# Optimization experiments

Measured on AMD Instinct MI355X. Metric: run time of the kernel, lower is better.

## Reference

```python
import jax, jax.numpy as jnp
import numpy as np

B, H, W, C = 8, 64, 64, 512
CK, CV = C // 8, C // 2  # 64, 256


def maxpool2x2(x):
    # x: [B, H, W, C] -> [B, H//2, W//2, C], 2x2 max pool, stride 2 (keras MaxPooling2D default)
    b, h, w, c = x.shape
    return x.reshape(b, h // 2, 2, w // 2, 2, c).max(axis=(2, 4))


def setup_inputs() -> dict:
    key = jax.random.key(0)
    ks = jax.random.split(key, 6)
    wscale = 0.02
    return {
        "x": jax.random.normal(ks[0], (B, H, W, C), dtype=jnp.float32),
        "w_theta": jax.random.normal(ks[1], (C, CK), dtype=jnp.float32) * wscale,
        "w_phi": jax.random.normal(ks[2], (C, CK), dtype=jnp.float32) * wscale,
        "w_g": jax.random.normal(ks[3], (C, CV), dtype=jnp.float32) * wscale,
        "w_o": jax.random.normal(ks[4], (CV, C), dtype=jnp.float32) * wscale,
        "gamma": jax.random.normal(ks[5], (1,), dtype=jnp.float32),
    }


def reference(x, w_theta, w_phi, w_g, w_o, gamma):
    b, h, w, c = x.shape
    hw = h * w
    # theta: 1x1 conv -> [B, HW, C//8]
    theta = jnp.einsum('bhwc,ck->bhwk', x, w_theta).reshape(b, hw, -1)
    # phi: 1x1 conv + 2x2 maxpool -> [B, HW//4, C//8]
    phi = maxpool2x2(jnp.einsum('bhwc,ck->bhwk', x, w_phi)).reshape(b, hw // 4, -1)
    # attention: [B, HW, HW//4], softmax over last axis
    attn = jax.nn.softmax(jnp.einsum('bqk,bpk->bqp', theta, phi), axis=-1)
    # g: 1x1 conv + 2x2 maxpool -> [B, HW//4, C//2]
    g = maxpool2x2(jnp.einsum('bhwc,cv->bhwv', x, w_g)).reshape(b, hw // 4, -1)
    # attn_g: [B, HW, C//2] -> [B, H, W, C//2] -> 1x1 conv -> [B, H, W, C]
    attn_g = jnp.einsum('bqp,bpv->bqv', attn, g).reshape(b, h, w, -1)
    attn_g = jnp.einsum('bhwv,vc->bhwc', attn_g, w_o)
    return x + gamma * attn_g
```

## Files before the change

### kernel.cpp

```cpp
#include <hip/hip_runtime.h>
#include <hip/hip_bf16.h>
#include <cstddef>
#include <cstdint>


typedef __attribute__((ext_vector_type(8))) short short8;
typedef __attribute__((ext_vector_type(4))) float float4v;

namespace {
constexpr int kB = 8, kC = 512, kCK = 64, kCV = 256, kHW = 4096, kP = 1024;
constexpr int kNP = 384;
}

__device__ __forceinline__ void gll16(const void* g, void* l) {
  __builtin_amdgcn_global_load_lds((uint32_t __attribute__((address_space(1)))*)g,
                                   (uint32_t __attribute__((address_space(3)))*)l,
                                   16, 0, 0);
}
__device__ __forceinline__ float4v mfma16(short8 a, short8 b, float4v c) {
  return __builtin_amdgcn_mfma_f32_16x16x32_bf16(a, b, c, 0, 0, 0);
}
__device__ __forceinline__ const short8* fragp(const char* tile, int row, int oct) {
  return (const short8*)(tile + row * 128 + ((oct ^ (row & 7)) * 16));
}
__device__ __forceinline__ const short8* fragp16(const char* tile, int row, int oct) {
  return (const short8*)(tile + row * 256 + ((oct ^ (row & 15)) * 16));
}

__global__ __launch_bounds__(256) void k_pack_w(
    const float* __restrict__ wt, const float* __restrict__ wphi,
    const float* __restrict__ wg, const float* __restrict__ wo,
    __hip_bfloat16* __restrict__ wAll, __hip_bfloat16* __restrict__ woT) {
  int idx = blockIdx.x * 256 + threadIdx.x;
  if (idx < 196608) {
    int n = idx >> 9, k = idx & 511;
    float v = (n < 64) ? wt[k * 64 + n]
            : (n < 128) ? wphi[k * 64 + (n - 64)]
                        : wg[k * 256 + (n - 128)];
    wAll[idx] = __float2bfloat16(v);
  } else {
    int t = idx - 196608;
    int n = t >> 8, k = t & 255;
    woT[t] = __float2bfloat16(wo[k * 512 + n]);
  }
}

__global__ __launch_bounds__(256) void k_proj(const float* __restrict__ x,
                                              const __hip_bfloat16* __restrict__ wAll,
                                              __hip_bfloat16* __restrict__ pgf) {
  __shared__ __align__(16) char smem[16384 + 49152];
  char* As = smem;
  char* Bs = smem + 16384;
  const int tid = threadIdx.x, wid = tid >> 6, lane = tid & 63;
  const int m = lane & 15, quad = lane >> 4;
  const int row0 = blockIdx.x * 64;
  const int wm = (wid >> 1) * 32, wn = (wid & 1) * 192;
  float4v acc[2][12] = {};
  for (int kc = 0; kc < 512; kc += 64) {
#pragma unroll
    for (int u = 0; u < 4; ++u) {
      const int r0 = (wid * 4 + u) * 4;
      const int row = r0 + (lane >> 4);
      const int sqg = (lane & 15) ^ (row & 15);
      gll16(x + (size_t)(row0 + row) * 512 + kc + sqg * 4, As + r0 * 256);
    }
#pragma unroll
    for (int u = 0; u < 12; ++u) {
      const int r0 = (wid * 12 + u) * 8;
      const int row = r0 + (lane >> 3);
      const int og = (lane & 7) ^ (row & 7);
      gll16(wAll + (size_t)row * 512 + kc + og * 8, Bs + r0 * 128);
    }
    __syncthreads();
#pragma unroll
    for (int kk = 0; kk < 64; kk += 32) {
      short8 af[2];
#pragma unroll
      for (int i = 0; i < 2; ++i) {
        const int row = wm + i * 16 + m;
        const int sq0 = (kk >> 2) + quad * 2;
        float4v lo = *(const float4v*)(As + row * 256 + ((sq0 ^ m) * 16));
        float4v hi = *(const float4v*)(As + row * 256 + (((sq0 + 1) ^ m) * 16));
        short8 a;
        a[0] = __builtin_bit_cast(short, __float2bfloat16(lo[0]));
        a[1] = __builtin_bit_cast(short, __float2bfloat16(lo[1]));
        a[2] = __builtin_bit_cast(short, __float2bfloat16(lo[2]));
        a[3] = __builtin_bit_cast(short, __float2bfloat16(lo[3]));
        a[4] = __builtin_bit_cast(short, __float2bfloat16(hi[0]));
        a[5] = __builtin_bit_cast(short, __float2bfloat16(hi[1]));
        a[6] = __builtin_bit_cast(short, __float2bfloat16(hi[2]));
        a[7] = __builtin_bit_cast(short, __float2bfloat16(hi[3]));
        af[i] = a;
      }
      const int oct = (kk >> 3) + quad;
#pragma unroll
      for (int j = 0; j < 12; ++j) {
        short8 bf = *fragp(Bs, wn + j * 16 + m, oct);
#pragma unroll
        for (int i = 0; i < 2; ++i) acc[i][j] = mfma16(af[i], bf, acc[i][j]);
      }
    }
    __syncthreads();
  }
#pragma unroll
  for (int i = 0; i < 2; ++i)
#pragma unroll
    for (int j = 0; j < 12; ++j)
#pragma unroll
      for (int r = 0; r < 4; ++r)
        pgf[(size_t)(row0 + wm + i * 16 + quad * 4 + r) * 384 + wn + j * 16 + m] =
            __float2bfloat16(acc[i][j][r]);
}

__global__ __launch_bounds__(256) void k_pool_phi(const __hip_bfloat16* __restrict__ pg,
                                                  __hip_bfloat16* __restrict__ phi_p) {
  int idx = blockIdx.x * 256 + threadIdx.x;
  int c = idx & 63;
  int p = (idx >> 6) & 1023;
  int b = idx >> 16;
  int ph = p >> 5, pw = p & 31;
  size_t base = ((size_t)b * 4096 + ph * 128 + pw * 2) * kNP + 64 + c;
  float v0 = __bfloat162float(pg[base]);
  float v1 = __bfloat162float(pg[base + kNP]);
  float v2 = __bfloat162float(pg[base + kNP * 64]);
  float v3 = __bfloat162float(pg[base + kNP * 64 + kNP]);
  phi_p[idx] = __float2bfloat16(fmaxf(fmaxf(v0, v1), fmaxf(v2, v3)));
}

__global__ __launch_bounds__(256) void k_pool_gT(const __hip_bfloat16* __restrict__ pg,
                                                 __hip_bfloat16* __restrict__ gT) {
  __shared__ __hip_bfloat16 t[64][65];
  const int p0 = blockIdx.x * 64, v0 = blockIdx.y * 64, b = blockIdx.z;
#pragma unroll
  for (int it = 0; it < 16; ++it) {
    int li = it * 256 + threadIdx.x;
    int pp = li >> 6, v = li & 63;
    int p = p0 + pp;
    int ph = p >> 5, pw = p & 31;
    size_t base = ((size_t)b * 4096 + ph * 128 + pw * 2) * kNP + 128 + v0 + v;
    float mv = fmaxf(
        fmaxf(__bfloat162float(pg[base]), __bfloat162float(pg[base + kNP])),
        fmaxf(__bfloat162float(pg[base + kNP * 64]), __bfloat162float(pg[base + kNP * 64 + kNP])));
    t[pp][v] = __float2bfloat16(mv);
  }
  __syncthreads();
#pragma unroll
  for (int it = 0; it < 16; ++it) {
    int li = it * 256 + threadIdx.x;
    int v = li >> 6, p = li & 63;
    gT[((size_t)b * 256 + v0 + v) * 1024 + p0 + p] = t[p][v];
  }
}

__global__ __launch_bounds__(512) void k_fattn(
    const __hip_bfloat16* __restrict__ pgf,
    const __hip_bfloat16* __restrict__ phip,
    const __hip_bfloat16* __restrict__ gT,
    __hip_bfloat16* __restrict__ O) {
  __shared__ __align__(16) char smem[65536 + 8192 + 1024 + 128];
  char* KG = smem;
  char* PQ = smem + 65536;
  float* pred = (float*)(smem + 65536 + 8192);
  float* rowstat = (float*)(smem + 65536 + 8192 + 1024);

  const int tid = threadIdx.x, wid = tid >> 6, lane = tid & 63;
  const int m = lane & 15, quad = lane >> 4;
  const int b = blockIdx.y, q0 = blockIdx.x * 32;

  if (wid < 4) {
    const int row = wid * 8 + (lane >> 3);
    const int og = (lane & 7) ^ (row & 7);
    gll16(pgf + (size_t)(b * kHW + q0 + row) * kNP + og * 8, PQ + wid * 8 * 128);
  }
  const __hip_bfloat16* phb = phip + (size_t)b * kP * 64;
  auto stageK = [&](int c, int buf) {
#pragma unroll
    for (int u = 0; u < 4; ++u) {
      const int r0 = wid * 32 + u * 8;
      const int row = r0 + (lane >> 3);
      const int og = (lane & 7) ^ (row & 7);
      gll16(phb + (size_t)(c * 256 + row) * 64 + og * 8, KG + buf * 32768 + r0 * 128);
    }
  };
  stageK(0, 0);
  __syncthreads();

  float4v sc[2][8] = {};
#pragma unroll
  for (int c = 0; c < 4; ++c) {
    if (c < 3) stageK(c + 1, (c + 1) & 1);
    const char* Kb = KG + (c & 1) * 32768;
    __builtin_amdgcn_s_setprio(1);
#pragma unroll
    for (int kk = 0; kk < 64; kk += 32) {
      const int oct = (kk >> 3) + quad;
      short8 a[2], bb[2];
#pragma unroll
      for (int i = 0; i < 2; ++i) a[i] = *fragp(PQ, i * 16 + m, oct);
#pragma unroll
      for (int j = 0; j < 2; ++j) bb[j] = *fragp(Kb, wid * 32 + j * 16 + m, oct);
#pragma unroll
      for (int i = 0; i < 2; ++i)
#pragma unroll
        for (int j = 0; j < 2; ++j) sc[i][c * 2 + j] = mfma16(a[i], bb[j], sc[i][c * 2 + j]);
    }
    __builtin_amdgcn_s_setprio(0);
    __syncthreads();
  }

  float mx[2][4];
#pragma unroll
  for (int i = 0; i < 2; ++i)
#pragma unroll
    for (int r = 0; r < 4; ++r) {
      float v = sc[i][0][r];
#pragma unroll
      for (int s = 1; s < 8; ++s) v = fmaxf(v, sc[i][s][r]);
#pragma unroll
      for (int d = 1; d < 16; d <<= 1) v = fmaxf(v, __shfl_xor(v, d));
      mx[i][r] = v;
    }
  if (m == 0) {
#pragma unroll
    for (int i = 0; i < 2; ++i)
#pragma unroll
      for (int r = 0; r < 4; ++r) pred[(i * 16 + quad * 4 + r) * 8 + wid] = mx[i][r];
  }
  __syncthreads();
  if (tid < 32) {
    float v = pred[tid * 8];
#pragma unroll
    for (int w = 1; w < 8; ++w) v = fmaxf(v, pred[tid * 8 + w]);
    rowstat[tid] = v;
  }
  __syncthreads();
  float sm[2][4];
#pragma unroll
  for (int i = 0; i < 2; ++i)
#pragma unroll
    for (int r = 0; r < 4; ++r) {
      const float rm = rowstat[i * 16 + quad * 4 + r];
      float s = 0.f;
#pragma unroll
      for (int ss = 0; ss < 8; ++ss) {
        float e = __expf(sc[i][ss][r] - rm);
        sc[i][ss][r] = e;
        s += e;
      }
#pragma unroll
      for (int d = 1; d < 16; d <<= 1) s += __shfl_xor(s, d);
      sm[i][r] = s;
    }
  __syncthreads();
  if (m == 0) {
#pragma unroll
    for (int i = 0; i < 2; ++i)
#pragma unroll
      for (int r = 0; r < 4; ++r) pred[(i * 16 + quad * 4 + r) * 8 + wid] = sm[i][r];
  }
  __syncthreads();
  if (tid < 32) {
    float s = 0.f;
#pragma unroll
    for (int w = 0; w < 8; ++w) s += pred[tid * 8 + w];
    rowstat[tid] = 1.f / s;
  }

  const __hip_bfloat16* gb = gT + (size_t)b * kCV * kP;
  auto stageG = [&](int cp, int buf) {
#pragma unroll
    for (int u = 0; u < 4; ++u) {
      const int r0 = wid * 32 + u * 8;
      const int row = r0 + (lane >> 3);
      const int og = (lane & 7) ^ (row & 7);
      gll16(gb + (size_t)row * kP + cp * 64 + og * 8, KG + buf * 32768 + r0 * 128);
    }
  };
  auto writePs = [&](int cp, int buf) {
    if ((wid >> 1) != (cp & 3)) return;
    const int c = cp >> 2;
    char* Pb = PQ + buf * 4096;
#pragma unroll
    for (int i = 0; i < 2; ++i)
#pragma unroll
      for (int jl = 0; jl < 2; ++jl) {
        const int pl = (wid & 1) * 32 + jl * 16 + m;
#pragma unroll
        for (int r = 0; r < 4; ++r) {
          const int row = i * 16 + quad * 4 + r;
          *(__hip_bfloat16*)(Pb + row * 128 + (((pl >> 3) ^ (row & 7)) * 16) +
                             (pl & 7) * 2) = __float2bfloat16(sc[i][c * 2 + jl][r]);
        }
      }
  };

  float4v oc[2][2] = {};
  stageG(0, 0);
  writePs(0, 0);
  __syncthreads();
  for (int cp = 0; cp < 16; ++cp) {
    const int cur = cp & 1;
    if (cp < 15) {
      stageG(cp + 1, cur ^ 1);
      writePs(cp + 1, cur ^ 1);
    }
    const char* Gb = KG + cur * 32768;
    const char* Pb = PQ + cur * 4096;
    __builtin_amdgcn_s_setprio(1);
#pragma unroll
    for (int kk = 0; kk < 64; kk += 32) {
      const int oct = (kk >> 3) + quad;
      short8 a[2], bb[2];
#pragma unroll
      for (int i = 0; i < 2; ++i) a[i] = *fragp(Pb, i * 16 + m, oct);
#pragma unroll
      for (int j = 0; j < 2; ++j) bb[j] = *fragp(Gb, wid * 32 + j * 16 + m, oct);
#pragma unroll
      for (int i = 0; i < 2; ++i)
#pragma unroll
        for (int j = 0; j < 2; ++j) oc[i][j] = mfma16(a[i], bb[j], oc[i][j]);
    }
    __builtin_amdgcn_s_setprio(0);
    __syncthreads();
  }
#pragma unroll
  for (int i = 0; i < 2; ++i)
#pragma unroll
    for (int j = 0; j < 2; ++j)
#pragma unroll
      for (int r = 0; r < 4; ++r) {
        const int row = i * 16 + quad * 4 + r;
        O[((size_t)b * kHW + q0 + row) * kCV + wid * 32 + j * 16 + m] =
            __float2bfloat16(oc[i][j][r] * rowstat[row]);
      }
}

__global__ __launch_bounds__(256) void k_out(const __hip_bfloat16* __restrict__ A,
                                             const __hip_bfloat16* __restrict__ Bw,
                                             const float* __restrict__ x,
                                             const float* __restrict__ gamma,
                                             float* __restrict__ out) {
  __shared__ __align__(16) char smem[4 * 16384];
  const int tid = threadIdx.x, wid = tid >> 6, lane = tid & 63;
  const int m = lane & 15, quad = lane >> 4;
  const int row0 = blockIdx.x * 128, col0 = blockIdx.y * 128;
  const int wm = (wid >> 1) * 64, wn = (wid & 1) * 64;
  float4v acc[4][4] = {};
  auto stage = [&](int t, int buf) {
    const int kc = t * 64;
#pragma unroll
    for (int u = 0; u < 4; ++u) {
      const int r0 = (wid * 4 + u) * 8;
      const int row = r0 + (lane >> 3);
      const int og = (lane & 7) ^ (row & 7);
      gll16(A + (size_t)(row0 + row) * 256 + kc + og * 8, smem + buf * 16384 + r0 * 128);
      gll16(Bw + (size_t)(col0 + row) * 256 + kc + og * 8,
            smem + 32768 + buf * 16384 + r0 * 128);
    }
  };
  stage(0, 0);
  __syncthreads();
#pragma unroll
  for (int t = 0; t < 4; ++t) {
    if (t < 3) stage(t + 1, (t + 1) & 1);
    const char* Ab = smem + (t & 1) * 16384;
    const char* Bb = smem + 32768 + (t & 1) * 16384;
    __builtin_amdgcn_s_setprio(1);
#pragma unroll
    for (int kk = 0; kk < 64; kk += 32) {
      const int oct = (kk >> 3) + quad;
      short8 af[4], bf[4];
#pragma unroll
      for (int i = 0; i < 4; ++i) af[i] = *fragp(Ab, wm + i * 16 + m, oct);
#pragma unroll
      for (int j = 0; j < 4; ++j) bf[j] = *fragp(Bb, wn + j * 16 + m, oct);
#pragma unroll
      for (int i = 0; i < 4; ++i)
#pragma unroll
        for (int j = 0; j < 4; ++j) acc[i][j] = mfma16(af[i], bf[j], acc[i][j]);
    }
    __builtin_amdgcn_s_setprio(0);
    __syncthreads();
  }
  const float g = gamma[0];
#pragma unroll
  for (int i = 0; i < 4; ++i)
#pragma unroll
    for (int j = 0; j < 4; ++j) {
      const int cc = col0 + wn + j * 16 + m;
      const int rb = row0 + wm + i * 16 + quad * 4;
#pragma unroll
      for (int r = 0; r < 4; ++r) {
        const size_t idx = (size_t)(rb + r) * 512 + cc;
        out[idx] = x[idx] + g * acc[i][j][r];
      }
    }
}

extern "C" void kernel_launch(void* const* d_in, const int* in_sizes, int n_in,
                              void* d_out, int out_size, void* d_ws, size_t ws_size,
                              hipStream_t stream) {
  (void)in_sizes; (void)n_in; (void)out_size; (void)ws_size;
  const float* x     = (const float*)d_in[0];
  const float* wt    = (const float*)d_in[1];
  const float* wphi  = (const float*)d_in[2];
  const float* wg    = (const float*)d_in[3];
  const float* wo    = (const float*)d_in[4];
  const float* gamma = (const float*)d_in[5];
  float* out = (float*)d_out;

  char* ws = (char*)d_ws;
  __hip_bfloat16* wAll = (__hip_bfloat16*)(ws);
  __hip_bfloat16* woT  = (__hip_bfloat16*)(ws + 393216);
  __hip_bfloat16* pgf  = (__hip_bfloat16*)(ws + 655360);
  __hip_bfloat16* phip = (__hip_bfloat16*)(ws + 25821184);
  __hip_bfloat16* gT   = (__hip_bfloat16*)(ws + 26869760);
  __hip_bfloat16* O    = (__hip_bfloat16*)(ws + 31064064);

  k_pack_w<<<1280, 256, 0, stream>>>(wt, wphi, wg, wo, wAll, woT);
  k_proj<<<512, 256, 0, stream>>>(x, wAll, pgf);
  k_pool_phi<<<2048, 256, 0, stream>>>(pgf, phip);
  k_pool_gT<<<dim3(16, 4, 8), 256, 0, stream>>>(pgf, gT);
  k_fattn<<<dim3(kHW / 32, kB), 512, 0, stream>>>(pgf, phip, gT, O);
  k_out<<<dim3(256, 4), 256, 0, stream>>>(O, woT, x, gamma, out);
}
```

Baseline: 237.9 us.

## Halve fused attention LDS footprint with smaller K/G tiles and register-held Q

```diff
diff --git a/kernel.cpp b/kernel.cpp
--- a/kernel.cpp
+++ b/kernel.cpp
@@ -23,8 +23,8 @@
 __device__ __forceinline__ const short8* fragp(const char* tile, int row, int oct) {
   return (const short8*)(tile + row * 128 + ((oct ^ (row & 7)) * 16));
 }
-__device__ __forceinline__ const short8* fragp16(const char* tile, int row, int oct) {
-  return (const short8*)(tile + row * 256 + ((oct ^ (row & 15)) * 16));
+__device__ __forceinline__ const short8* fragp4(const char* tile, int row, int oct) {
+  return (const short8*)(tile + row * 64 + ((oct ^ (row & 3)) * 16));
 }
 
 __global__ __launch_bounds__(256) void k_pack_w(
@@ -157,11 +157,11 @@
     const __hip_bfloat16* __restrict__ phip,
     const __hip_bfloat16* __restrict__ gT,
     __hip_bfloat16* __restrict__ O) {
-  __shared__ __align__(16) char smem[65536 + 8192 + 1024 + 128];
+  __shared__ __align__(16) char smem[32768 + 4096];
   char* KG = smem;
-  char* PQ = smem + 65536;
-  float* pred = (float*)(smem + 65536 + 8192);
-  float* rowstat = (float*)(smem + 65536 + 8192 + 1024);
+  char* PQ = smem + 32768;
+  float* pred = (float*)(KG + 16384);
+  float* rowstat = (float*)(KG + 16384 + 1024);
 
   const int tid = threadIdx.x, wid = tid >> 6, lane = tid & 63;
   const int m = lane & 15, quad = lane >> 4;
@@ -175,34 +175,33 @@
   const __hip_bfloat16* phb = phip + (size_t)b * kP * 64;
   auto stageK = [&](int c, int buf) {
 #pragma unroll
-    for (int u = 0; u < 4; ++u) {
-      const int r0 = wid * 32 + u * 8;
+    for (int u = 0; u < 2; ++u) {
+      const int r0 = wid * 16 + u * 8;
       const int row = r0 + (lane >> 3);
       const int og = (lane & 7) ^ (row & 7);
-      gll16(phb + (size_t)(c * 256 + row) * 64 + og * 8, KG + buf * 32768 + r0 * 128);
+      gll16(phb + (size_t)(c * 128 + row) * 64 + og * 8, KG + buf * 16384 + r0 * 128);
     }
   };
   stageK(0, 0);
   __syncthreads();
 
+  short8 aq[2][2];
+#pragma unroll
+  for (int i = 0; i < 2; ++i)
+#pragma unroll
+    for (int t = 0; t < 2; ++t) aq[i][t] = *fragp(PQ, i * 16 + m, t * 4 + quad);
+
   float4v sc[2][8] = {};
 #pragma unroll
-  for (int c = 0; c < 4; ++c) {
-    if (c < 3) stageK(c + 1, (c + 1) & 1);
-    const char* Kb = KG + (c & 1) * 32768;
+  for (int c = 0; c < 8; ++c) {
+    if (c < 7) stageK(c + 1, (c + 1) & 1);
+    const char* Kb = KG + (c & 1) * 16384;
     __builtin_amdgcn_s_setprio(1);
 #pragma unroll
-    for (int kk = 0; kk < 64; kk += 32) {
-      const int oct = (kk >> 3) + quad;
-      short8 a[2], bb[2];
-#pragma unroll
-      for (int i = 0; i < 2; ++i) a[i] = *fragp(PQ, i * 16 + m, oct);
-#pragma unroll
-      for (int j = 0; j < 2; ++j) bb[j] = *fragp(Kb, wid * 32 + j * 16 + m, oct);
-#pragma unroll
-      for (int i = 0; i < 2; ++i)
-#pragma unroll
-        for (int j = 0; j < 2; ++j) sc[i][c * 2 + j] = mfma16(a[i], bb[j], sc[i][c * 2 + j]);
+    for (int t = 0; t < 2; ++t) {
+      short8 bb = *fragp(Kb, wid * 16 + m, t * 4 + quad);
+#pragma unroll
+      for (int i = 0; i < 2; ++i) sc[i][c] = mfma16(aq[i][t], bb, sc[i][c]);
     }
     __builtin_amdgcn_s_setprio(0);
     __syncthreads();
@@ -265,61 +264,72 @@
     for (int w = 0; w < 8; ++w) s += pred[tid * 8 + w];
     rowstat[tid] = 1.f / s;
   }
+  __syncthreads();
+  float rinv[2][4];
+#pragma unroll
+  for (int i = 0; i < 2; ++i)
+#pragma unroll
+    for (int r = 0; r < 4; ++r) rinv[i][r] = rowstat[i * 16 + quad * 4 + r];
+  __syncthreads();
 
   const __hip_bfloat16* gb = gT + (size_t)b * kCV * kP;
   auto stageG = [&](int cp, int buf) {
 #pragma unroll
-    for (int u = 0; u < 4; ++u) {
-      const int r0 = wid * 32 + u * 8;
-      const int row = r0 + (lane >> 3);
-      const int og = (lane & 7) ^ (row & 7);
-      gll16(gb + (size_t)row * kP + cp * 64 + og * 8, KG + buf * 32768 + r0 * 128);
+    for (int u = 0; u < 2; ++u) {
+      const int r0 = wid * 32 + u * 16;
+      const int row = r0 + (lane >> 2);
+      const int og = (lane & 3) ^ (row & 3);
+      gll16(gb + (size_t)row * kP + cp * 32 + og * 8, KG + buf * 16384 + r0 * 64);
     }
   };
-  auto writePs = [&](int cp, int buf) {
-    if ((wid >> 1) != (cp & 3)) return;
-    const int c = cp >> 2;
-    char* Pb = PQ + buf * 4096;
-#pragma unroll
-    for (int i = 0; i < 2; ++i)
-#pragma unroll
-      for (int jl = 0; jl < 2; ++jl) {
-        const int pl = (wid & 1) * 32 + jl * 16 + m;
+
+  float4v oc[2][2] = {};
+  stageG(0, 0);
+  {
+    if ((wid >> 1) == 0) {
+      const int pl = (wid & 1) * 16 + m;
+#pragma unroll
+      for (int i = 0; i < 2; ++i)
 #pragma unroll
         for (int r = 0; r < 4; ++r) {
           const int row = i * 16 + quad * 4 + r;
-          *(__hip_bfloat16*)(Pb + row * 128 + (((pl >> 3) ^ (row & 7)) * 16) +
-                             (pl & 7) * 2) = __float2bfloat16(sc[i][c * 2 + jl][r]);
+          *(__hip_bfloat16*)(PQ + row * 64 + (((pl >> 3) ^ (row & 3)) * 16) +
+                             (pl & 7) * 2) = __float2bfloat16(sc[i][0][r]);
         }
-      }
-  };
-
-  float4v oc[2][2] = {};
-  stageG(0, 0);
-  writePs(0, 0);
-  __syncthreads();
-  for (int cp = 0; cp < 16; ++cp) {
+    }
+  }
+  __syncthreads();
+#pragma unroll
+  for (int cp = 0; cp < 32; ++cp) {
     const int cur = cp & 1;
-    if (cp < 15) {
+    if (cp < 31) {
       stageG(cp + 1, cur ^ 1);
-      writePs(cp + 1, cur ^ 1);
-    }
-    const char* Gb = KG + cur * 32768;
-    const char* Pb = PQ + cur * 4096;
+      if ((wid >> 1) == ((cp + 1) & 3)) {
+        const int c = (cp + 1) >> 2;
+        const int pl = (wid & 1) * 16 + m;
+        char* Pb = PQ + (cur ^ 1) * 2048;
+#pragma unroll
+        for (int i = 0; i < 2; ++i)
+#pragma unroll
+          for (int r = 0; r < 4; ++r) {
+            const int row = i * 16 + quad * 4 + r;
+            *(__hip_bfloat16*)(Pb + row * 64 + (((pl >> 3) ^ (row & 3)) * 16) +
+                               (pl & 7) * 2) = __float2bfloat16(sc[i][c][r]);
+          }
+      }
+    }
+    const char* Gb = KG + cur * 16384;
+    const char* Pb = PQ + cur * 2048;
     __builtin_amdgcn_s_setprio(1);
-#pragma unroll
-    for (int kk = 0; kk < 64; kk += 32) {
-      const int oct = (kk >> 3) + quad;
-      short8 a[2], bb[2];
-#pragma unroll
-      for (int i = 0; i < 2; ++i) a[i] = *fragp(Pb, i * 16 + m, oct);
-#pragma unroll
-      for (int j = 0; j < 2; ++j) bb[j] = *fragp(Gb, wid * 32 + j * 16 + m, oct);
-#pragma unroll
-      for (int i = 0; i < 2; ++i)
-#pragma unroll
-        for (int j = 0; j < 2; ++j) oc[i][j] = mfma16(a[i], bb[j], oc[i][j]);
-    }
+    short8 a[2], bb[2];
+#pragma unroll
+    for (int i = 0; i < 2; ++i) a[i] = *fragp4(Pb, i * 16 + m, quad);
+#pragma unroll
+    for (int j = 0; j < 2; ++j) bb[j] = *fragp4(Gb, wid * 32 + j * 16 + m, quad);
+#pragma unroll
+    for (int i = 0; i < 2; ++i)
+#pragma unroll
+      for (int j = 0; j < 2; ++j) oc[i][j] = mfma16(a[i], bb[j], oc[i][j]);
     __builtin_amdgcn_s_setprio(0);
     __syncthreads();
   }
@@ -331,7 +341,7 @@
       for (int r = 0; r < 4; ++r) {
         const int row = i * 16 + quad * 4 + r;
         O[((size_t)b * kHW + q0 + row) * kCV + wid * 32 + j * 16 + m] =
-            __float2bfloat16(oc[i][j][r] * rowstat[row]);
+            __float2bfloat16(oc[i][j][r] * rinv[i][r]);
       }
 }
 
```

Result: slower. 251.0 us (+5.5%).
